# Performance work log

Measured on AMD Instinct MI355X. Metric: run time of the kernel, lower is better.

The kernel has to match this reference:

```python
import jax, jax.numpy as jnp
import numpy as np

EMB = 1024
H = 16
D = EMB // H  # 64
EPS = 1e-5
SM_SCALE = 1.0  # forward default sm_scale=1.0
CAUSAL = True
NEG = -1e30


def _layernorm(t, g, b):
    # LayerNorm over last dim (head_dim), per torch nn.LayerNorm(head_dim)
    m = jnp.mean(t, axis=-1, keepdims=True)
    v = jnp.mean(jnp.square(t - m), axis=-1, keepdims=True)
    return (t - m) * jax.lax.rsqrt(v + EPS) * g + b


def setup_inputs() -> dict:
    key = jax.random.key(0)
    ks = jax.random.split(key, 8)
    N, L = 2, 2048
    x = jax.random.normal(ks[0], (N, L, EMB), dtype=jnp.float32)
    mask = jnp.ones((N, L), dtype=jnp.int32)  # accepted but unused, as in the torch module
    s = 0.02
    Wq = jax.random.normal(ks[1], (EMB, EMB), dtype=jnp.float32) * s
    Wk = jax.random.normal(ks[2], (EMB, EMB), dtype=jnp.float32) * s
    Wv = jax.random.normal(ks[3], (EMB, EMB), dtype=jnp.float32) * s
    Wo = jax.random.normal(ks[4], (EMB, EMB), dtype=jnp.float32) * s
    bo = jnp.zeros((EMB,), dtype=jnp.float32)
    gq = jnp.ones((D,), dtype=jnp.float32)
    bq = jnp.zeros((D,), dtype=jnp.float32)
    gk = jnp.ones((D,), dtype=jnp.float32)
    bk = jnp.zeros((D,), dtype=jnp.float32)
    return {"x": x, "mask": mask, "Wq": Wq, "Wk": Wk, "Wv": Wv,
            "gq": gq, "bq": bq, "gk": gk, "bk": bk, "Wo": Wo, "bo": bo}


def reference(x, mask, Wq, Wk, Wv, gq, bq, gk, bk, Wo, bo):
    N, L, _ = x.shape
    # QKV projections (torch Linear: x @ W.T), split into heads -> [N, H, L, D]
    q = (x @ Wq.T).reshape(N, L, H, D).transpose(0, 2, 1, 3)
    k = (x @ Wk.T).reshape(N, L, H, D).transpose(0, 2, 1, 3)
    v = (x @ Wv.T).reshape(N, L, H, D).transpose(0, 2, 1, 3)
    # fused_q_norm variant: per-head LayerNorm on Q and K (fused into attention kernel)
    q = _layernorm(q, gq, bq)
    k = _layernorm(k, gk, bk)
    scores = jnp.einsum('nhld,nhmd->nhlm', q, k) * SM_SCALE  # [N,H,L,L]
    if CAUSAL:
        causal = jnp.tril(jnp.ones((L, L), dtype=bool))
        scores = jnp.where(causal, scores, NEG)
    attn = jax.nn.softmax(scores, axis=-1)
    out = jnp.einsum('nhlm,nhmd->nhld', attn, v)
    out = out.transpose(0, 2, 1, 3).reshape(N, L, EMB)
    return out @ Wo.T + bo
```

## Files before the change

kernel.cpp:

```cpp
#include <hip/hip_runtime.h>
#include <stdint.h>

typedef unsigned short u16;
typedef u16   u16x4    __attribute__((ext_vector_type(4)));
typedef u16   u16x8    __attribute__((ext_vector_type(8)));
typedef u16x8 u16x8_ma __attribute__((may_alias));
typedef __bf16 bf16x8  __attribute__((ext_vector_type(8)));
typedef float f32x4    __attribute__((ext_vector_type(4)));
typedef f32x4 f32x4_ma __attribute__((may_alias));

#define EMB    1024
#define NHEAD  16
#define HD     64
#define SEQ    2048
#define NBATCH 2
#define ROWS   (NBATCH*SEQ)
#define SATT   72

__device__ __forceinline__ u16 f2b(float f) {
  uint32_t u; __builtin_memcpy(&u, &f, 4);
  u = u + 0x7fffu + ((u >> 16) & 1u);
  return (u16)(u >> 16);
}
__device__ __forceinline__ u16x8 ld8(const u16* p) { return *(const u16x8_ma*)p; }
__device__ __forceinline__ void  st8(u16* p, u16x8 v) { *(u16x8_ma*)p = v; }
__device__ __forceinline__ bf16x8 asbf(u16x8 v) {
  union { u16x8 u; bf16x8 b; } c; c.u = v; return c.b;
}
__device__ __forceinline__ void async_cp16(const u16* g, u16* l) {
  __builtin_amdgcn_global_load_lds(
      (const __attribute__((address_space(1))) void*)g,
      (__attribute__((address_space(3))) void*)l, 16, 0, 0);
}

__global__ __launch_bounds__(256) void cvt_all(
    const float* __restrict__ x,
    const float* __restrict__ w0, const float* __restrict__ w1,
    const float* __restrict__ w2, const float* __restrict__ w3,
    u16* __restrict__ xd, u16* __restrict__ d0, u16* __restrict__ d1,
    u16* __restrict__ d2, u16* __restrict__ d3)
{
  int bid = blockIdx.x;
  const float* s; u16* d; int off;
  if (bid < 4096) { s = x; d = xd; off = bid; }
  else {
    int t = bid - 4096; int m = t >> 10; off = t & 1023;
    switch (m) {
      case 0: s = w0; d = d0; break;
      case 1: s = w1; d = d1; break;
      case 2: s = w2; d = d2; break;
      default: s = w3; d = d3; break;
    }
  }
  size_t i = ((size_t)off * 256 + threadIdx.x) * 4;
  f32x4 v = *(const f32x4_ma*)(s + i);
  u16x4 o;
  #pragma unroll
  for (int j = 0; j < 4; j++) o[j] = f2b(v[j]);
  *(u16x4*)(d + i) = o;
}

template<int AMODE>
__device__ __forceinline__ void gemm_acc_128x128(
    const u16* __restrict__ A, const u16* __restrict__ B,
    int m0, int n0, u16* As, u16* Bs, f32x4 acc[4][4])
{
  const int tid  = threadIdx.x;
  const int lane = tid & 63;
  const int wave = tid >> 6;
  const int wm   = (wave >> 1) * 64;
  const int wn   = (wave & 1) * 64;
  const int ar   = tid >> 2;
  const int ac   = (tid & 3) * 8;
  const int lm   = lane & 15;
  const int lk   = (lane >> 4) * 8;

  #pragma unroll
  for (int i = 0; i < 4; i++)
    #pragma unroll
    for (int j = 0; j < 4; j++)
      #pragma unroll
      for (int e = 0; e < 4; e++) acc[i][j][e] = 0.f;

  for (int k0 = 0; k0 < EMB; k0 += 64) {
    size_t a0[2], a1[2];
    #pragma unroll
    for (int pnl = 0; pnl < 2; pnl++) {
      int kc = k0 + pnl * 32 + ac;
      if (AMODE == 0) {
        a0[pnl] = (size_t)(m0 + ar)      * EMB + kc;
        a1[pnl] = (size_t)(m0 + ar + 64) * EMB + kc;
      } else {
        int h = kc >> 6, d = kc & 63;
        int r0 = m0 + ar, r1 = m0 + ar + 64;
        a0[pnl] = (((size_t)((r0 >> 11) * NHEAD + h)) * SEQ + (r0 & (SEQ-1))) * HD + d;
        a1[pnl] = (((size_t)((r1 >> 11) * NHEAD + h)) * SEQ + (r1 & (SEQ-1))) * HD + d;
      }
    }
    __syncthreads();
    #pragma unroll
    for (int pnl = 0; pnl < 2; pnl++) {
      const int pb = pnl * 4096;
      async_cp16(A + a0[pnl], As + pb + tid * 8);
      async_cp16(A + a1[pnl], As + pb + (tid + 256) * 8);
      async_cp16(B + (size_t)(n0 + ar)      * EMB + k0 + pnl * 32 + ac, Bs + pb + tid * 8);
      async_cp16(B + (size_t)(n0 + ar + 64) * EMB + k0 + pnl * 32 + ac, Bs + pb + (tid + 256) * 8);
    }
    __syncthreads();

    #pragma unroll
    for (int pnl = 0; pnl < 2; pnl++) {
      const int pb = pnl * 4096;
      bf16x8 af[4], bfr[4];
      #pragma unroll
      for (int i = 0; i < 4; i++)
        af[i] = asbf(ld8(As + pb + (wm + i * 16 + lm) * 32 + lk));
      #pragma unroll
      for (int j = 0; j < 4; j++)
        bfr[j] = asbf(ld8(Bs + pb + (wn + j * 16 + lm) * 32 + lk));
      #pragma unroll
      for (int i = 0; i < 4; i++)
        #pragma unroll
        for (int j = 0; j < 4; j++)
          acc[i][j] = __builtin_amdgcn_mfma_f32_16x16x32_bf16(af[i], bfr[j], acc[i][j], 0, 0, 0);
    }
  }
}

__device__ __forceinline__ void epilogue_scatter_ln(
    f32x4 acc[4][4], u16* dst, int m0, int n0, int head_base, int Hdst,
    const float* g, const float* b, int do_ln)
{
  const int lane = threadIdx.x & 63, wave = threadIdx.x >> 6;
  const int wm = (wave >> 1) * 64, wn = (wave & 1) * 64;
  const int lm = lane & 15, quad = lane >> 4;

  float gv[4], bv[4];
  #pragma unroll
  for (int j = 0; j < 4; j++) { gv[j] = g[j * 16 + lm]; bv[j] = b[j * 16 + lm]; }

  #pragma unroll
  for (int i = 0; i < 4; i++)
    #pragma unroll
    for (int r = 0; r < 4; r++) {
      float val[4];
      #pragma unroll
      for (int j = 0; j < 4; j++) val[j] = acc[i][j][r];
      if (do_ln) {
        float s = val[0] + val[1] + val[2] + val[3];
        #pragma unroll
        for (int o = 8; o >= 1; o >>= 1) s += __shfl_xor(s, o, 64);
        float mean = s * (1.f / 64.f);
        float ss = 0.f;
        #pragma unroll
        for (int j = 0; j < 4; j++) { val[j] -= mean; ss += val[j] * val[j]; }
        #pragma unroll
        for (int o = 8; o >= 1; o >>= 1) ss += __shfl_xor(ss, o, 64);
        float inv = rsqrtf(ss * (1.f / 64.f) + 1e-5f);
        #pragma unroll
        for (int j = 0; j < 4; j++) val[j] = val[j] * inv * gv[j] + bv[j];
      }
      int row = m0 + wm + i * 16 + quad * 4 + r;
      int bn = row >> 11, l = row & (SEQ - 1);
      #pragma unroll
      for (int j = 0; j < 4; j++) {
        int col = n0 + wn + j * 16 + lm;
        int hl = (col >> 6) - head_base, d = col & 63;
        dst[(((size_t)(bn * Hdst + hl)) * SEQ + l) * HD + d] = f2b(val[j]);
      }
    }
}

__global__ __launch_bounds__(256) void gemm_qkv(
    const u16* __restrict__ x,
    const u16* __restrict__ Wq, const u16* __restrict__ Wk, const u16* __restrict__ Wv,
    const float* __restrict__ gq, const float* __restrict__ bq,
    const float* __restrict__ gk, const float* __restrict__ bk,
    u16* __restrict__ qd, u16* __restrict__ kb, u16* __restrict__ vb)
{
  __shared__ __align__(16) u16 As[128 * 64];
  __shared__ __align__(16) u16 Bs[128 * 64];
  const u16* W; u16* dst; const float* g; const float* b; int ln;
  if (blockIdx.z == 0)      { W = Wq; dst = qd; g = gq; b = bq; ln = 1; }
  else if (blockIdx.z == 1) { W = Wk; dst = kb; g = gk; b = bk; ln = 1; }
  else                      { W = Wv; dst = vb; g = gq; b = bq; ln = 0; }
  const int m0 = blockIdx.y * 128, n0 = blockIdx.x * 128;
  f32x4 acc[4][4];
  gemm_acc_128x128<0>(x, W, m0, n0, As, Bs, acc);
  epilogue_scatter_ln(acc, dst, m0, n0, 0, NHEAD, g, b, ln);
}

__global__ __launch_bounds__(256) void gemm_q(
    const u16* __restrict__ x, const u16* __restrict__ Wq,
    const float* __restrict__ gq, const float* __restrict__ bq,
    u16* __restrict__ qd)
{
  __shared__ __align__(16) u16 As[128 * 64];
  __shared__ __align__(16) u16 Bs[128 * 64];
  const int m0 = blockIdx.y * 128, n0 = blockIdx.x * 128;
  f32x4 acc[4][4];
  gemm_acc_128x128<0>(x, Wq, m0, n0, As, Bs, acc);
  epilogue_scatter_ln(acc, qd, m0, n0, 0, NHEAD, gq, bq, 1);
}
__global__ __launch_bounds__(256) void gemm_kv(
    const u16* __restrict__ x,
    const u16* __restrict__ Wk, const u16* __restrict__ Wv,
    const float* __restrict__ gk, const float* __restrict__ bk,
    u16* __restrict__ k, u16* __restrict__ v, int head_lo, int hpp)
{
  __shared__ __align__(16) u16 As[128 * 64];
  __shared__ __align__(16) u16 Bs[128 * 64];
  const int m0 = blockIdx.y * 128, n0 = blockIdx.x * 128;
  const u16* W = (blockIdx.z == 0 ? Wk : Wv) + (size_t)head_lo * HD * EMB;
  u16* dst = (blockIdx.z == 0) ? k : v;
  f32x4 acc[4][4];
  gemm_acc_128x128<0>(x, W, m0, n0, As, Bs, acc);
  epilogue_scatter_ln(acc, dst, m0, n0, 0, hpp, gk, bk, blockIdx.z == 0);
}

__global__ __launch_bounds__(256) void attn(
    u16* qd, const u16* __restrict__ K, const u16* __restrict__ V,
    int head_lo, int hpp)
{
  __shared__ __align__(16) u16 Ks[2][64 * SATT];
  __shared__ __align__(16) u16 Vts[2][64 * 64];
  __shared__ __align__(16) u16 Ps[4][16 * SATT];

  const int p = blockIdx.x, hl = blockIdx.y, n = blockIdx.z;
  const int qa = p, qb = 31 - p;
  const int tid = threadIdx.x, lane = tid & 63, wave = tid >> 6;
  const int lm = lane & 15, quad = lane >> 4, lk = quad * 8;
  u16* Qh = qd + ((size_t)(n * NHEAD + head_lo + hl)) * SEQ * HD;
  const u16* Kh = K + ((size_t)(n * hpp + hl)) * SEQ * HD;
  const u16* Vh = V + ((size_t)(n * hpp + hl)) * SEQ * HD;

  const int sr = tid >> 3;
  const int sc = (tid & 7) * 8;
  const int vswz = tid & 7;

  bf16x8 aqA[2], aqB[2];
  #pragma unroll
  for (int ks = 0; ks < 2; ++ks) {
    aqA[ks] = asbf(ld8(Qh + (size_t)(qa * 64 + wave * 16 + lm) * HD + ks * 32 + lk));
    aqB[ks] = asbf(ld8(Qh + (size_t)(qb * 64 + wave * 16 + lm) * HD + ks * 32 + lk));
  }

  u16x8 kr0, kr1, vr0, vr1;
  kr0 = ld8(Kh + (size_t)(sr)      * HD + sc);
  kr1 = ld8(Kh + (size_t)(sr + 32) * HD + sc);
  vr0 = ld8(Vh + (size_t)(sr)      * HD + sc);
  vr1 = ld8(Vh + (size_t)(sr + 32) * HD + sc);
  st8(&Ks[0][sr * SATT + sc], kr0);
  st8(&Ks[0][(sr + 32) * SATT + sc], kr1);
  #pragma unroll
  for (int jj = 0; jj < 8; jj++) {
    int d = sc + jj;
    Vts[0][d * 64 + (((sr >> 3) ^ vswz) * 8) + (sr & 7)]        = vr0[jj];
    Vts[0][d * 64 + ((((sr + 32) >> 3) ^ vswz) * 8) + (sr & 7)] = vr1[jj];
  }
  kr0 = ld8(Kh + (size_t)(64 + sr)      * HD + sc);
  kr1 = ld8(Kh + (size_t)(64 + sr + 32) * HD + sc);
  vr0 = ld8(Vh + (size_t)(64 + sr)      * HD + sc);
  vr1 = ld8(Vh + (size_t)(64 + sr + 32) * HD + sc);
  __syncthreads();

  f32x4 oA[4], oB[4];
  float mA[4], psA[4], mB[4], psB[4];
  #pragma unroll
  for (int j = 0; j < 4; j++)
    #pragma unroll
    for (int e = 0; e < 4; e++) { oA[j][e] = 0.f; oB[j][e] = 0.f; }
  #pragma unroll
  for (int r = 0; r < 4; r++) { mA[r] = -1e30f; psA[r] = 0.f; mB[r] = -1e30f; psB[r] = 0.f; }

  u16* Pw = &Ps[wave][0];

  for (int t = 0; t <= qb; ++t) {
    const int cur = t & 1;
    if (t < qb) {
      const int nb = 1 - cur;
      st8(&Ks[nb][sr * SATT + sc], kr0);
      st8(&Ks[nb][(sr + 32) * SATT + sc], kr1);
      #pragma unroll
      for (int jj = 0; jj < 8; jj++) {
        int d = sc + jj;
        Vts[nb][d * 64 + (((sr >> 3) ^ vswz) * 8) + (sr & 7)]        = vr0[jj];
        Vts[nb][d * 64 + ((((sr + 32) >> 3) ^ vswz) * 8) + (sr & 7)] = vr1[jj];
      }
      if (t + 1 < qb) {
        const size_t base = (size_t)(t + 2) * 64;
        kr0 = ld8(Kh + (base + sr)      * HD + sc);
        kr1 = ld8(Kh + (base + sr + 32) * HD + sc);
        vr0 = ld8(Vh + (base + sr)      * HD + sc);
        vr1 = ld8(Vh + (base + sr + 32) * HD + sc);
      }
    }

    #pragma unroll
    for (int tile = 0; tile < 2; ++tile) {
      if (tile == 1 && t > qa) break;
      const int qx = tile ? qa : qb;
      bf16x8* aq = tile ? aqA : aqB;
      f32x4*  oacc = tile ? oA : oB;
      float*  m_i = tile ? mA : mB;
      float*  psum = tile ? psA : psB;

      f32x4 s[4];
      #pragma unroll
      for (int j = 0; j < 4; j++)
        #pragma unroll
        for (int e = 0; e < 4; e++) s[j][e] = 0.f;
      #pragma unroll
      for (int ks = 0; ks < 2; ++ks)
        #pragma unroll
        for (int j = 0; j < 4; j++) {
          bf16x8 bk = asbf(ld8(&Ks[cur][(j * 16 + lm) * SATT + ks * 32 + lk]));
          s[j] = __builtin_amdgcn_mfma_f32_16x16x32_bf16(aq[ks], bk, s[j], 0, 0, 0);
        }
      if (t == qx) {
        #pragma unroll
        for (int j = 0; j < 4; j++) {
          int col = t * 64 + j * 16 + lm;
          #pragma unroll
          for (int r = 0; r < 4; r++) {
            int row = qx * 64 + wave * 16 + quad * 4 + r;
            if (col > row) s[j][r] = -1e30f;
          }
        }
      }
      float mnew[4], alpha[4], part[4];
      #pragma unroll
      for (int r = 0; r < 4; r++) {
        float mx = fmaxf(fmaxf(s[0][r], s[1][r]), fmaxf(s[2][r], s[3][r]));
        #pragma unroll
        for (int o = 8; o >= 1; o >>= 1) mx = fmaxf(mx, __shfl_xor(mx, o, 64));
        mnew[r] = fmaxf(m_i[r], mx);
        alpha[r] = __expf(m_i[r] - mnew[r]);
        m_i[r] = mnew[r];
        part[r] = 0.f;
      }
      #pragma unroll
      for (int j = 0; j < 4; j++)
        #pragma unroll
        for (int r = 0; r < 4; r++) {
          float pv = __expf(s[j][r] - mnew[r]);
          s[j][r] = pv;
          part[r] += pv;
        }
      #pragma unroll
      for (int r = 0; r < 4; r++) psum[r] = psum[r] * alpha[r] + part[r];
      #pragma unroll
      for (int j = 0; j < 4; j++)
        #pragma unroll
        for (int r = 0; r < 4; r++) oacc[j][r] *= alpha[r];

      #pragma unroll
      for (int j = 0; j < 4; j++)
        #pragma unroll
        for (int r = 0; r < 4; r++)
          Pw[(quad * 4 + r) * SATT + j * 16 + lm] = f2b(s[j][r]);
      __asm__ __volatile__("" ::: "memory");

      #pragma unroll
      for (int ks = 0; ks < 2; ++ks) {
        bf16x8 ap = asbf(ld8(Pw + lm * SATT + ks * 32 + lk));
        #pragma unroll
        for (int j = 0; j < 4; j++) {
          int dg = 2 * j + (lm >> 3);
          int g  = (ks * 4 + quad) ^ (dg & 7);
          bf16x8 bv = asbf(ld8(&Vts[cur][(j * 16 + lm) * 64 + g * 8]));
          oacc[j] = __builtin_amdgcn_mfma_f32_16x16x32_bf16(ap, bv, oacc[j], 0, 0, 0);
        }
      }
    }
    __syncthreads();
  }

  #pragma unroll
  for (int r = 0; r < 4; r++) {
    float sA = psA[r], sB = psB[r];
    #pragma unroll
    for (int o = 8; o >= 1; o >>= 1) { sA += __shfl_xor(sA, o, 64); sB += __shfl_xor(sB, o, 64); }
    float invA = 1.0f / sA, invB = 1.0f / sB;
    int rowA = qa * 64 + wave * 16 + quad * 4 + r;
    int rowB = qb * 64 + wave * 16 + quad * 4 + r;
    #pragma unroll
    for (int j = 0; j < 4; j++) {
      Qh[(size_t)rowB * HD + j * 16 + lm] = f2b(oB[j][r] * invB);
      Qh[(size_t)rowA * HD + j * 16 + lm] = f2b(oA[j][r] * invA);
    }
  }
}

__global__ __launch_bounds__(256) void gemm_out(
    const u16* __restrict__ ao, const u16* __restrict__ Wo,
    const float* __restrict__ bo, float* __restrict__ out)
{
  __shared__ __align__(16) u16 As[64 * 64];
  __shared__ __align__(16) u16 Bs[128 * 64];
  const int m0 = blockIdx.y * 64, n0 = blockIdx.x * 128;
  const int tid  = threadIdx.x;
  const int lane = tid & 63;
  const int wave = tid >> 6;
  const int wm   = (wave >> 1) * 32;
  const int wn   = (wave & 1) * 64;
  const int ar   = tid >> 2;
  const int ac   = (tid & 3) * 8;
  const int lm   = lane & 15;
  const int lk   = (lane >> 4) * 8;

  f32x4 acc[2][4];
  #pragma unroll
  for (int i = 0; i < 2; i++)
    #pragma unroll
    for (int j = 0; j < 4; j++)
      #pragma unroll
      for (int e = 0; e < 4; e++) acc[i][j][e] = 0.f;

  for (int k0 = 0; k0 < EMB; k0 += 64) {
    size_t aoff[2];
    #pragma unroll
    for (int pnl = 0; pnl < 2; pnl++) {
      int kc = k0 + pnl * 32 + ac, h = kc >> 6, d = kc & 63;
      int r0 = m0 + ar;
      aoff[pnl] = (((size_t)((r0 >> 11) * NHEAD + h)) * SEQ + (r0 & (SEQ-1))) * HD + d;
    }
    __syncthreads();
    #pragma unroll
    for (int pnl = 0; pnl < 2; pnl++) {
      async_cp16(ao + aoff[pnl], As + pnl * 2048 + tid * 8);
      async_cp16(Wo + (size_t)(n0 + ar)      * EMB + k0 + pnl * 32 + ac, Bs + pnl * 4096 + tid * 8);
      async_cp16(Wo + (size_t)(n0 + ar + 64) * EMB + k0 + pnl * 32 + ac, Bs + pnl * 4096 + (tid + 256) * 8);
    }
    __syncthreads();

    #pragma unroll
    for (int pnl = 0; pnl < 2; pnl++) {
      bf16x8 af[2], bfr[4];
      #pragma unroll
      for (int i = 0; i < 2; i++)
        af[i] = asbf(ld8(As + pnl * 2048 + (wm + i * 16 + lm) * 32 + lk));
      #pragma unroll
      for (int j = 0; j < 4; j++)
        bfr[j] = asbf(ld8(Bs + pnl * 4096 + (wn + j * 16 + lm) * 32 + lk));
      #pragma unroll
      for (int i = 0; i < 2; i++)
        #pragma unroll
        for (int j = 0; j < 4; j++)
          acc[i][j] = __builtin_amdgcn_mfma_f32_16x16x32_bf16(af[i], bfr[j], acc[i][j], 0, 0, 0);
    }
  }

  const int quad = lane >> 4;
  #pragma unroll
  for (int j = 0; j < 4; j++) {
    int col = n0 + wn + j * 16 + lm;
    float bias = bo[col];
    #pragma unroll
    for (int i = 0; i < 2; i++)
      #pragma unroll
      for (int r = 0; r < 4; r++) {
        int row = m0 + wm + i * 16 + quad * 4 + r;
        out[(size_t)row * EMB + col] = acc[i][j][r] + bias;
      }
  }
}

extern "C" void kernel_launch(void* const* d_in, const int* in_sizes, int n_in,
                              void* d_out, int out_size, void* d_ws, size_t ws_size,
                              hipStream_t stream)
{
  const float* xf  = (const float*)d_in[0];
  const float* Wqf = (const float*)d_in[2];
  const float* Wkf = (const float*)d_in[3];
  const float* Wvf = (const float*)d_in[4];
  const float* gq  = (const float*)d_in[5];
  const float* bq  = (const float*)d_in[6];
  const float* gk  = (const float*)d_in[7];
  const float* bk  = (const float*)d_in[8];
  const float* Wof = (const float*)d_in[9];
  const float* bo  = (const float*)d_in[10];

  const size_t MB = 1u << 20;
  u16* xb  = (u16*)d_ws;
  u16* wqb = xb  + (size_t)ROWS * EMB;
  u16* wkb = wqb + (size_t)EMB * EMB;
  u16* wvb = wkb + (size_t)EMB * EMB;
  u16* wob = wvb + (size_t)EMB * EMB;
  u16* kvbase = wob + (size_t)EMB * EMB;

  size_t avail = (ws_size > 16 * MB) ? ws_size - 16 * MB : 2 * MB;
  int hpp = NHEAD;
  while ((size_t)hpp * MB > avail && hpp > 2) hpp >>= 1;
  const size_t kv_elems = (size_t)hpp * NBATCH * SEQ * HD;
  u16* kbuf = kvbase;
  u16* vbuf = kbuf + kv_elems;

  u16* qd = (u16*)d_in[0];
  float* out = (float*)d_out;

  cvt_all<<<dim3(8192), 256, 0, stream>>>(xf, Wqf, Wkf, Wvf, Wof,
                                          xb, wqb, wkb, wvb, wob);
  if (hpp == NHEAD) {
    gemm_qkv<<<dim3(8, 32, 3), 256, 0, stream>>>(xb, wqb, wkb, wvb,
                                                 gq, bq, gk, bk,
                                                 qd, kbuf, vbuf);
    attn<<<dim3(16, NHEAD, NBATCH), 256, 0, stream>>>(qd, kbuf, vbuf, 0, NHEAD);
  } else {
    gemm_q<<<dim3(8, 32), 256, 0, stream>>>(xb, wqb, gq, bq, qd);
    for (int g = 0; g < NHEAD / hpp; ++g) {
      gemm_kv<<<dim3(hpp / 2, 32, 2), 256, 0, stream>>>(xb, wkb, wvb, gk, bk,
                                                        kbuf, vbuf, g * hpp, hpp);
      attn<<<dim3(16, hpp, NBATCH), 256, 0, stream>>>(qd, kbuf, vbuf, g * hpp, hpp);
    }
  }
  gemm_out<<<dim3(8, 64), 256, 0, stream>>>(qd, wob, bo, out);
}
```

Before: 228.5 us.

## Restructure attention to one query tile per block with register-resident P

Attention blocks now each handle a single 64-row query tile instead of a paired causal tile (qa, 31-p), doubling the grid and using a permuted tile-to-block mapping for balance. The QK^T MFMA operands are swapped so scores come out transposed, which lets the row-max and sum reductions use just two cross-lane shuffles. P is converted with packed bf16 conversion and redistributed through ds_bpermute rather than an LDS scratch buffer, removing the Ps shared array. The change also adds s_setprio around the MFMA sections and a launch_bounds occupancy hint. It aims to cut LDS traffic and raise occupancy, at the cost of losing the paired-tile load balance and adding more blocks with uneven work.

```diff
diff --git a/kernel.cpp b/kernel.cpp
--- a/kernel.cpp
+++ b/kernel.cpp
@@ -26,6 +26,11 @@
 __device__ __forceinline__ void  st8(u16* p, u16x8 v) { *(u16x8_ma*)p = v; }
 __device__ __forceinline__ bf16x8 asbf(u16x8 v) {
   union { u16x8 u; bf16x8 b; } c; c.u = v; return c.b;
+}
+__device__ __forceinline__ uint32_t cvtpk(float a, float b) {
+  uint32_t r;
+  asm("v_cvt_pk_bf16_f32 %0, %1, %2" : "=v"(r) : "v"(a), "v"(b));
+  return r;
 }
 __device__ __forceinline__ void async_cp16(const u16* g, u16* l) {
   __builtin_amdgcn_global_load_lds(
@@ -218,16 +223,15 @@
   epilogue_scatter_ln(acc, dst, m0, n0, 0, hpp, gk, bk, blockIdx.z == 0);
 }
 
-__global__ __launch_bounds__(256) void attn(
+__global__ __launch_bounds__(256, 4) void attn(
     u16* qd, const u16* __restrict__ K, const u16* __restrict__ V,
     int head_lo, int hpp)
 {
   __shared__ __align__(16) u16 Ks[2][64 * SATT];
   __shared__ __align__(16) u16 Vts[2][64 * 64];
-  __shared__ __align__(16) u16 Ps[4][16 * SATT];
-
-  const int p = blockIdx.x, hl = blockIdx.y, n = blockIdx.z;
-  const int qa = p, qb = 31 - p;
+
+  const int hl = blockIdx.y, n = blockIdx.z;
+  const int p = (7 * blockIdx.x + hl + 16 * n) & 31;
   const int tid = threadIdx.x, lane = tid & 63, wave = tid >> 6;
   const int lm = lane & 15, quad = lane >> 4, lk = quad * 8;
   u16* Qh = qd + ((size_t)(n * NHEAD + head_lo + hl)) * SEQ * HD;
@@ -238,12 +242,10 @@
   const int sc = (tid & 7) * 8;
   const int vswz = tid & 7;
 
-  bf16x8 aqA[2], aqB[2];
-  #pragma unroll
-  for (int ks = 0; ks < 2; ++ks) {
-    aqA[ks] = asbf(ld8(Qh + (size_t)(qa * 64 + wave * 16 + lm) * HD + ks * 32 + lk));
-    aqB[ks] = asbf(ld8(Qh + (size_t)(qb * 64 + wave * 16 + lm) * HD + ks * 32 + lk));
-  }
+  bf16x8 aq[2];
+  #pragma unroll
+  for (int ks = 0; ks < 2; ++ks)
+    aq[ks] = asbf(ld8(Qh + (size_t)(p * 64 + wave * 16 + lm) * HD + ks * 32 + lk));
 
   u16x8 kr0, kr1, vr0, vr1;
   kr0 = ld8(Kh + (size_t)(sr)      * HD + sc);
@@ -264,20 +266,20 @@
   vr1 = ld8(Vh + (size_t)(64 + sr + 32) * HD + sc);
   __syncthreads();
 
-  f32x4 oA[4], oB[4];
-  float mA[4], psA[4], mB[4], psB[4];
+  f32x4 oacc[4];
   #pragma unroll
   for (int j = 0; j < 4; j++)
     #pragma unroll
-    for (int e = 0; e < 4; e++) { oA[j][e] = 0.f; oB[j][e] = 0.f; }
-  #pragma unroll
-  for (int r = 0; r < 4; r++) { mA[r] = -1e30f; psA[r] = 0.f; mB[r] = -1e30f; psB[r] = 0.f; }
-
-  u16* Pw = &Ps[wave][0];
-
-  for (int t = 0; t <= qb; ++t) {
+    for (int e = 0; e < 4; e++) oacc[j][e] = 0.f;
+  float m_i = -1e30f, psum = 0.f;
+
+  const int idx0 = (((quad & 1) * 2) * 16 + lm) * 4;
+  const int idx1 = idx0 + 64;
+  const int qrow = p * 64 + wave * 16 + lm;
+
+  for (int t = 0; t <= p; ++t) {
     const int cur = t & 1;
-    if (t < qb) {
+    if (t < p) {
       const int nb = 1 - cur;
       st8(&Ks[nb][sr * SATT + sc], kr0);
       st8(&Ks[nb][(sr + 32) * SATT + sc], kr1);
@@ -287,7 +289,7 @@
         Vts[nb][d * 64 + (((sr >> 3) ^ vswz) * 8) + (sr & 7)]        = vr0[jj];
         Vts[nb][d * 64 + ((((sr + 32) >> 3) ^ vswz) * 8) + (sr & 7)] = vr1[jj];
       }
-      if (t + 1 < qb) {
+      if (t + 1 < p) {
         const size_t base = (size_t)(t + 2) * 64;
         kr0 = ld8(Kh + (base + sr)      * HD + sc);
         kr1 = ld8(Kh + (base + sr + 32) * HD + sc);
@@ -296,99 +298,104 @@
       }
     }
 
-    #pragma unroll
-    for (int tile = 0; tile < 2; ++tile) {
-      if (tile == 1 && t > qa) break;
-      const int qx = tile ? qa : qb;
-      bf16x8* aq = tile ? aqA : aqB;
-      f32x4*  oacc = tile ? oA : oB;
-      float*  m_i = tile ? mA : mB;
-      float*  psum = tile ? psA : psB;
-
-      f32x4 s[4];
+    f32x4 s[4];
+    #pragma unroll
+    for (int j = 0; j < 4; j++)
+      #pragma unroll
+      for (int e = 0; e < 4; e++) s[j][e] = 0.f;
+    __builtin_amdgcn_s_setprio(1);
+    #pragma unroll
+    for (int ks = 0; ks < 2; ++ks)
+      #pragma unroll
+      for (int j = 0; j < 4; j++) {
+        bf16x8 ak = asbf(ld8(&Ks[cur][(j * 16 + lm) * SATT + ks * 32 + lk]));
+        s[j] = __builtin_amdgcn_mfma_f32_16x16x32_bf16(ak, aq[ks], s[j], 0, 0, 0);
+      }
+    __builtin_amdgcn_s_setprio(0);
+
+    if (t == p) {
       #pragma unroll
       for (int j = 0; j < 4; j++)
         #pragma unroll
-        for (int e = 0; e < 4; e++) s[j][e] = 0.f;
-      #pragma unroll
-      for (int ks = 0; ks < 2; ++ks)
-        #pragma unroll
-        for (int j = 0; j < 4; j++) {
-          bf16x8 bk = asbf(ld8(&Ks[cur][(j * 16 + lm) * SATT + ks * 32 + lk]));
-          s[j] = __builtin_amdgcn_mfma_f32_16x16x32_bf16(aq[ks], bk, s[j], 0, 0, 0);
-        }
-      if (t == qx) {
-        #pragma unroll
-        for (int j = 0; j < 4; j++) {
-          int col = t * 64 + j * 16 + lm;
-          #pragma unroll
-          for (int r = 0; r < 4; r++) {
-            int row = qx * 64 + wave * 16 + quad * 4 + r;
-            if (col > row) s[j][r] = -1e30f;
-          }
-        }
-      }
-      float mnew[4], alpha[4], part[4];
+        for (int r = 0; r < 4; r++)
+          if (t * 64 + j * 16 + quad * 4 + r > qrow) s[j][r] = -1e30f;
+    }
+
+    float mx = fmaxf(fmaxf(s[0][0], s[0][1]), fmaxf(s[0][2], s[0][3]));
+    #pragma unroll
+    for (int j = 1; j < 4; j++)
+      mx = fmaxf(mx, fmaxf(fmaxf(s[j][0], s[j][1]), fmaxf(s[j][2], s[j][3])));
+    mx = fmaxf(mx, __shfl_xor(mx, 16, 64));
+    mx = fmaxf(mx, __shfl_xor(mx, 32, 64));
+    const float mnew = fmaxf(m_i, mx);
+    const float alpha = __expf(m_i - mnew);
+    m_i = mnew;
+    float part = 0.f;
+    #pragma unroll
+    for (int j = 0; j < 4; j++)
       #pragma unroll
       for (int r = 0; r < 4; r++) {
-        float mx = fmaxf(fmaxf(s[0][r], s[1][r]), fmaxf(s[2][r], s[3][r]));
-        #pragma unroll
-        for (int o = 8; o >= 1; o >>= 1) mx = fmaxf(mx, __shfl_xor(mx, o, 64));
-        mnew[r] = fmaxf(m_i[r], mx);
-        alpha[r] = __expf(m_i[r] - mnew[r]);
-        m_i[r] = mnew[r];
-        part[r] = 0.f;
-      }
-      #pragma unroll
-      for (int j = 0; j < 4; j++)
-        #pragma unroll
-        for (int r = 0; r < 4; r++) {
-          float pv = __expf(s[j][r] - mnew[r]);
-          s[j][r] = pv;
-          part[r] += pv;
-        }
-      #pragma unroll
-      for (int r = 0; r < 4; r++) psum[r] = psum[r] * alpha[r] + part[r];
-      #pragma unroll
-      for (int j = 0; j < 4; j++)
-        #pragma unroll
-        for (int r = 0; r < 4; r++) oacc[j][r] *= alpha[r];
-
-      #pragma unroll
-      for (int j = 0; j < 4; j++)
-        #pragma unroll
-        for (int r = 0; r < 4; r++)
-          Pw[(quad * 4 + r) * SATT + j * 16 + lm] = f2b(s[j][r]);
-      __asm__ __volatile__("" ::: "memory");
-
-      #pragma unroll
-      for (int ks = 0; ks < 2; ++ks) {
-        bf16x8 ap = asbf(ld8(Pw + lm * SATT + ks * 32 + lk));
-        #pragma unroll
-        for (int j = 0; j < 4; j++) {
-          int dg = 2 * j + (lm >> 3);
-          int g  = (ks * 4 + quad) ^ (dg & 7);
-          bf16x8 bv = asbf(ld8(&Vts[cur][(j * 16 + lm) * 64 + g * 8]));
-          oacc[j] = __builtin_amdgcn_mfma_f32_16x16x32_bf16(ap, bv, oacc[j], 0, 0, 0);
-        }
-      }
-    }
+        float pv = __expf(s[j][r] - mnew);
+        s[j][r] = pv;
+        part += pv;
+      }
+    psum = psum * alpha + part;
+
+    float ar_[4];
+    #pragma unroll
+    for (int r = 0; r < 4; r++)
+      ar_[r] = __shfl(alpha, (lane & 48) | (quad * 4 + r), 64);
+    #pragma unroll
+    for (int j = 0; j < 4; j++)
+      #pragma unroll
+      for (int r = 0; r < 4; r++) oacc[j][r] *= ar_[r];
+
+    uint32_t u[8];
+    #pragma unroll
+    for (int j = 0; j < 4; j++) {
+      u[2 * j]     = cvtpk(s[j][0], s[j][1]);
+      u[2 * j + 1] = cvtpk(s[j][2], s[j][3]);
+    }
+
+    __builtin_amdgcn_s_setprio(1);
+    #pragma unroll
+    for (int ks = 0; ks < 2; ++ks) {
+      union { uint32_t w[4]; bf16x8 v; } cv;
+      #pragma unroll
+      for (int w = 0; w < 4; w++) {
+        int lo = __builtin_amdgcn_ds_bpermute(w < 2 ? idx0 : idx1,
+                                              (int)u[ks * 4 + (w & 1)]);
+        int hi = __builtin_amdgcn_ds_bpermute(w < 2 ? idx0 : idx1,
+                                              (int)u[ks * 4 + 2 + (w & 1)]);
+        cv.w[w] = (quad < 2) ? (uint32_t)lo : (uint32_t)hi;
+      }
+      bf16x8 ap = cv.v;
+      #pragma unroll
+      for (int j = 0; j < 4; j++) {
+        int dg = 2 * j + (lm >> 3);
+        int g  = (ks * 4 + quad) ^ (dg & 7);
+        bf16x8 bv = asbf(ld8(&Vts[cur][(j * 16 + lm) * 64 + g * 8]));
+        oacc[j] = __builtin_amdgcn_mfma_f32_16x16x32_bf16(ap, bv, oacc[j], 0, 0, 0);
+      }
+    }
+    __builtin_amdgcn_s_setprio(0);
     __syncthreads();
   }
 
+  float s_ = psum;
+  s_ += __shfl_xor(s_, 16, 64);
+  s_ += __shfl_xor(s_, 32, 64);
+  const float inv = 1.0f / s_;
+  float ir_[4];
+  #pragma unroll
+  for (int r = 0; r < 4; r++)
+    ir_[r] = __shfl(inv, (lane & 48) | (quad * 4 + r), 64);
   #pragma unroll
   for (int r = 0; r < 4; r++) {
-    float sA = psA[r], sB = psB[r];
-    #pragma unroll
-    for (int o = 8; o >= 1; o >>= 1) { sA += __shfl_xor(sA, o, 64); sB += __shfl_xor(sB, o, 64); }
-    float invA = 1.0f / sA, invB = 1.0f / sB;
-    int rowA = qa * 64 + wave * 16 + quad * 4 + r;
-    int rowB = qb * 64 + wave * 16 + quad * 4 + r;
-    #pragma unroll
-    for (int j = 0; j < 4; j++) {
-      Qh[(size_t)rowB * HD + j * 16 + lm] = f2b(oB[j][r] * invB);
-      Qh[(size_t)rowA * HD + j * 16 + lm] = f2b(oA[j][r] * invA);
-    }
+    const int row = p * 64 + wave * 16 + quad * 4 + r;
+    #pragma unroll
+    for (int j = 0; j < 4; j++)
+      Qh[(size_t)row * HD + j * 16 + lm] = f2b(oacc[j][r] * ir_[r]);
   }
 }
 
@@ -505,13 +512,13 @@
     gemm_qkv<<<dim3(8, 32, 3), 256, 0, stream>>>(xb, wqb, wkb, wvb,
                                                  gq, bq, gk, bk,
                                                  qd, kbuf, vbuf);
-    attn<<<dim3(16, NHEAD, NBATCH), 256, 0, stream>>>(qd, kbuf, vbuf, 0, NHEAD);
+    attn<<<dim3(32, NHEAD, NBATCH), 256, 0, stream>>>(qd, kbuf, vbuf, 0, NHEAD);
   } else {
     gemm_q<<<dim3(8, 32), 256, 0, stream>>>(xb, wqb, gq, bq, qd);
     for (int g = 0; g < NHEAD / hpp; ++g) {
       gemm_kv<<<dim3(hpp / 2, 32, 2), 256, 0, stream>>>(xb, wkb, wvb, gk, bk,
                                                         kbuf, vbuf, g * hpp, hpp);
-      attn<<<dim3(16, hpp, NBATCH), 256, 0, stream>>>(qd, kbuf, vbuf, g * hpp, hpp);
+      attn<<<dim3(32, hpp, NBATCH), 256, 0, stream>>>(qd, kbuf, vbuf, g * hpp, hpp);
     }
   }
   gemm_out<<<dim3(8, 64), 256, 0, stream>>>(qd, wob, bo, out);
```

New measurement: 225.5 us. Within noise of the previous version (-1.3%).
